# Kernel optimization log

Measured on AMD Instinct MI355X. Metric: run time of the kernel, lower is better.

Reference implementation:

```python
import jax, jax.numpy as jnp
import numpy as np
from jax import lax


def _log_g(z):
    # log of g(x) = x + 0.5 if x >= 0 else sigmoid(x)
    return jnp.where(z >= 0, jnp.log(jax.nn.relu(z) + 0.5), -jax.nn.softplus(-z))


def setup_inputs() -> dict:
    key = jax.random.key(0)
    k1, k2, k3 = jax.random.split(key, 3)
    B, S, D, H = 8, 8192, 512, 256
    x = jax.random.normal(k1, (B, S, D), dtype=jnp.float32)
    h_prev = jax.random.normal(k2, (B, H), dtype=jnp.float32)
    # nn.Linear(D, 3H, bias=False) weight: [3H, D], scaled like torch default init
    W = jax.random.normal(k3, (3 * H, D), dtype=jnp.float32) * (1.0 / np.sqrt(D))
    return {"x": x, "h_prev": h_prev, "W": W}


def reference(x, h_prev, W):
    # x: [B,S,D], h_prev: [B,H], W: [3H,D]
    seq_len = x.shape[1]
    y = jnp.einsum("bsd,hd->bsh", x, W)              # [B,S,3H]
    f, i, h = jnp.split(y, 3, axis=-1)                # each [B,S,H]
    diff = jax.nn.softplus(-f) - jax.nn.softplus(-i)
    log_f = -jax.nn.softplus(diff)                    # log(sigmoid-normalized forget gate)
    log_i = -jax.nn.softplus(-diff)                   # log(input gate)
    log_h0 = _log_g(h_prev)                           # [B,H]
    log_tilde_h = _log_g(h)                           # [B,S,H]
    # parallel scan in log space: h_t = f_t * h_{t-1} + i_t * g(h_t~)
    a_star = jnp.concatenate(
        [jnp.zeros_like(log_h0)[:, None], jnp.cumsum(log_f, axis=1)], axis=1
    )                                                  # [B,S+1,H]
    log_vals = jnp.concatenate([log_h0[:, None], log_i + log_tilde_h], axis=1)  # [B,S+1,H]
    log_h = a_star + lax.cumlogsumexp(log_vals - a_star, axis=1)
    h_t = jnp.exp(log_h)                               # [B,S+1,H]
    return h_t[:, -seq_len:]                           # [B,S,H]
```

## Files before the change

kernel.cpp:

```cpp
#include <hip/hip_runtime.h>
#include <hip/hip_fp16.h>
#include <math.h>

#define BB 8
#define SS 8192
#define DD 512
#define HH 256
#define MM (BB * SS)
#define NN 768
#define CC 256
#define LL 32

typedef unsigned short u16;
typedef __attribute__((ext_vector_type(8))) short short8;
typedef __attribute__((ext_vector_type(4))) float f32x4;

#define AS1(p) ((const __attribute__((address_space(1))) void*)(p))
#define AS3(p) ((__attribute__((address_space(3))) void*)(p))

__device__ __forceinline__ u16 f2bf_rtne(float f) {
    union { float f; unsigned u; } v; v.f = f;
    unsigned r = v.u + 0x7fffu + ((v.u >> 16) & 1u);
    return (u16)(r >> 16);
}
__device__ __forceinline__ unsigned pack2_rtn(float a, float b) {
    union { float f; unsigned u; } x, y; x.f = a; y.f = b;
    return ((x.u + 0x8000u) >> 16) | ((y.u + 0x8000u) & 0xffff0000u);
}

__device__ __forceinline__ float sp_fast(float z) {
    return (z > 15.0f) ? z : __logf(1.0f + __expf(z));
}

__device__ __forceinline__ unsigned packFu(float F, float u) {
    __half2 h = __floats2half2_rn(F, u);
    return *reinterpret_cast<unsigned*>(&h);
}
__device__ __forceinline__ float2 unpackFu(unsigned v) {
    __half2 h = *reinterpret_cast<__half2*>(&v);
    return __half22float2(h);
}

__global__ __launch_bounds__(256) void convert_W(const float* __restrict__ W,
                                                 u16* __restrict__ Wr) {
    const int chunk = blockIdx.x * 256 + threadIdx.x;
    const int kcb = chunk / 768;
    const int u = chunk % 768;
    const int kc = kcb >> 2, cb = kcb & 3;
    const int v = u & 31;
    const int s = ((v >> 2) & 7) ^ ((v >> 4) & 1);
    const int q = (v & 3) ^ (s & 3);
    const int r = ((u >> 5) << 3) | s;
    const int w = r / 48;
    const int rr = r % 48;
    const int jn = rr >> 4, hl = rr & 15;
    const int wrow = jn * HH + cb * 64 + w * 16 + hl;
    const int k0 = kc * 32 + q * 8;
    const float4 v0 = *(const float4*)&W[(size_t)wrow * DD + k0];
    const float4 v1 = *(const float4*)&W[(size_t)wrow * DD + k0 + 4];
    u16 o[8];
    o[0]=f2bf_rtne(v0.x); o[1]=f2bf_rtne(v0.y); o[2]=f2bf_rtne(v0.z); o[3]=f2bf_rtne(v0.w);
    o[4]=f2bf_rtne(v1.x); o[5]=f2bf_rtne(v1.y); o[6]=f2bf_rtne(v1.z); o[7]=f2bf_rtne(v1.w);
    *(uint4*)&Wr[(size_t)chunk * 8] = *(const uint4*)o;
}

__global__ __launch_bounds__(256, 4) void gemm_gate_mfma(
    const float* __restrict__ x,
    const u16* __restrict__ Wr,
    unsigned* __restrict__ Fu)
{
    __shared__ __align__(16) u16 Bs[2][6144];
    __shared__ __align__(16) u16 As[2][64 * 40];

    const int tid = threadIdx.x;
    const int L = (blockIdx.x & 7) * 512 + (blockIdx.x >> 3);
    const int mblk = L >> 2, cb = L & 3;
    const int m0 = mblk * 64;

    const int w = tid >> 6;
    const int lane = tid & 63;
    const int l16 = lane & 15;
    const int quad = lane >> 4;

    const int arow = tid >> 2;
    const int aqi = tid & 3;

    f32x4 acc[4][3];
    #pragma unroll
    for (int a = 0; a < 4; ++a)
        #pragma unroll
        for (int b = 0; b < 3; ++b)
            #pragma unroll
            for (int e = 0; e < 4; ++e) acc[a][b][e] = 0.0f;

    int boff[3];
    #pragma unroll
    for (int jn = 0; jn < 3; ++jn) {
        const int r = w * 48 + jn * 16 + l16;
        boff[jn] = (((r * 4 + quad) ^ (r & 7))) * 8;
    }

    const float* xrow = &x[(size_t)(m0 + arow) * DD];

    {
        const size_t ub = (size_t)(0 * 4 + cb) * 768;
        #pragma unroll
        for (int i = 0; i < 3; ++i) {
            const int idx = i * 256 + tid;
            __builtin_amdgcn_global_load_lds(AS1(Wr + (ub + idx) * 8),
                                             AS3(&Bs[0][idx * 8]), 16, 0, 0);
        }
    }
    float4 va0 = *(const float4*)&xrow[aqi * 8];
    float4 va1 = *(const float4*)&xrow[aqi * 8 + 4];
    float4 ar0 = *(const float4*)&xrow[32 + aqi * 8];
    float4 ar1 = *(const float4*)&xrow[32 + aqi * 8 + 4];
    {
        uint4 p;
        p.x = pack2_rtn(va0.x, va0.y); p.y = pack2_rtn(va0.z, va0.w);
        p.z = pack2_rtn(va1.x, va1.y); p.w = pack2_rtn(va1.z, va1.w);
        *(uint4*)&As[0][arow * 40 + aqi * 8] = p;
    }
    __syncthreads();

    for (int kc = 0; kc < 16; ++kc) {
        const int buf = kc & 1;
        if (kc < 15) {
            const size_t ub = (size_t)((kc + 1) * 4 + cb) * 768;
            #pragma unroll
            for (int i = 0; i < 3; ++i) {
                const int idx = i * 256 + tid;
                __builtin_amdgcn_global_load_lds(AS1(Wr + (ub + idx) * 8),
                                                 AS3(&Bs[buf ^ 1][idx * 8]), 16, 0, 0);
            }
            uint4 p;
            p.x = pack2_rtn(ar0.x, ar0.y); p.y = pack2_rtn(ar0.z, ar0.w);
            p.z = pack2_rtn(ar1.x, ar1.y); p.w = pack2_rtn(ar1.z, ar1.w);
            *(uint4*)&As[buf ^ 1][arow * 40 + aqi * 8] = p;
            if (kc < 14) {
                ar0 = *(const float4*)&xrow[(kc + 2) * 32 + aqi * 8];
                ar1 = *(const float4*)&xrow[(kc + 2) * 32 + aqi * 8 + 4];
            }
        }
        short8 afr[4];
        #pragma unroll
        for (int mf = 0; mf < 4; ++mf)
            afr[mf] = *(const short8*)&As[buf][(mf * 16 + l16) * 40 + quad * 8];
        short8 bfr[3];
        #pragma unroll
        for (int jn = 0; jn < 3; ++jn)
            bfr[jn] = *(const short8*)&Bs[buf][boff[jn]];

        __builtin_amdgcn_s_setprio(1);
        #pragma unroll
        for (int mf = 0; mf < 4; ++mf)
            #pragma unroll
            for (int jn = 0; jn < 3; ++jn)
                acc[mf][jn] = __builtin_amdgcn_mfma_f32_16x16x32_bf16(
                    afr[mf], bfr[jn], acc[mf][jn], 0, 0, 0);
        __builtin_amdgcn_s_setprio(0);
        __syncthreads();
    }

    const int head = cb * 64 + w * 16 + l16;
    #pragma unroll
    for (int mf = 0; mf < 4; ++mf) {
        #pragma unroll
        for (int r = 0; r < 4; ++r) {
            const int m = m0 + mf * 16 + quad * 4 + r;
            const float fr = acc[mf][0][r];
            const float ir = acc[mf][1][r];
            const float hr = acc[mf][2][r];
            const float diff = sp_fast(-fr) - sp_fast(-ir);
            const float F = __builtin_amdgcn_rcpf(1.0f + __expf(diff));
            const float I = 1.0f - F;
            const float G = (hr >= 0.0f) ? (hr + 0.5f)
                                         : __builtin_amdgcn_rcpf(1.0f + __expf(-hr));
            Fu[(size_t)m * HH + head] = packFu(F, I * G);
        }
    }
}

__global__ __launch_bounds__(256) void scan_pass1(
    const unsigned* __restrict__ Fu,
    float* __restrict__ P_arr, float* __restrict__ U_arr) {
    const int pair = blockIdx.x * 2 + (threadIdx.x >> 7);
    const int b = pair / CC;
    const int c = pair % CC;
    const int h0 = (threadIdx.x & 127) * 2;
    size_t base = ((size_t)(b * SS + c * LL)) * HH + h0;
    float P0 = 1.0f, P1 = 1.0f, U0 = 0.0f, U1 = 0.0f;
    #pragma unroll 8
    for (int t = 0; t < LL; ++t) {
        const uint2 fu = *(const uint2*)&Fu[base];
        const float2 a = unpackFu(fu.x);
        const float2 d = unpackFu(fu.y);
        U0 = a.x * U0 + a.y;  P0 *= a.x;
        U1 = d.x * U1 + d.y;  P1 *= d.x;
        base += HH;
    }
    const size_t o = ((size_t)c * BB + b) * HH + h0;
    *(float2*)&P_arr[o] = make_float2(P0, P1);
    *(float2*)&U_arr[o] = make_float2(U0, U1);
}

__global__ __launch_bounds__(256) void scan_pass2(
    const float* __restrict__ h_prev, const float* __restrict__ P_arr,
    const float* __restrict__ U_arr, float* __restrict__ Hin) {
    const int b = blockIdx.x;
    const int h = threadIdx.x;
    const float z = h_prev[b * HH + h];
    float carry = (z >= 0.0f) ? (z + 0.5f) : __builtin_amdgcn_rcpf(1.0f + __expf(-z));
    #pragma unroll 8
    for (int c = 0; c < CC; ++c) {
        const size_t o = ((size_t)c * BB + b) * HH + h;
        Hin[o] = carry;
        carry = P_arr[o] * carry + U_arr[o];
    }
}

__global__ __launch_bounds__(256) void scan_pass3(
    const float* __restrict__ Hin, unsigned* buf) {
    const int pair = blockIdx.x * 2 + (threadIdx.x >> 7);
    const int b = pair / CC;
    const int c = pair % CC;
    const int h0 = (threadIdx.x & 127) * 2;
    float2 hv = *(const float2*)&Hin[((size_t)c * BB + b) * HH + h0];
    size_t base = ((size_t)(b * SS + c * LL)) * HH + h0;
    #pragma unroll 8
    for (int t = 0; t < LL; ++t) {
        const uint2 fu = *(const uint2*)&buf[base];
        const float2 a = unpackFu(fu.x);
        const float2 d = unpackFu(fu.y);
        hv.x = a.x * hv.x + a.y;
        hv.y = d.x * hv.y + d.y;
        *(float2*)&buf[base] = hv;
        base += HH;
    }
}

extern "C" void kernel_launch(void* const* d_in, const int* in_sizes, int n_in,
                              void* d_out, int out_size, void* d_ws, size_t ws_size,
                              hipStream_t stream) {
    const float* x      = (const float*)d_in[0];
    const float* h_prev = (const float*)d_in[1];
    const float* W      = (const float*)d_in[2];

    float* P_arr = (float*)d_ws;
    float* U_arr = P_arr + (size_t)CC * BB * HH;
    float* Hin   = U_arr + (size_t)CC * BB * HH;
    u16*   Wr    = (u16*)(Hin + (size_t)CC * BB * HH);

    convert_W<<<192, 256, 0, stream>>>(W, Wr);
    gemm_gate_mfma<<<4096, 256, 0, stream>>>(x, Wr, (unsigned*)d_out);
    scan_pass1<<<BB * CC / 2, 256, 0, stream>>>((const unsigned*)d_out, P_arr, U_arr);
    scan_pass2<<<BB, 256, 0, stream>>>(h_prev, P_arr, U_arr, Hin);
    scan_pass3<<<BB * CC / 2, 256, 0, stream>>>(Hin, (unsigned*)d_out);
}
```

Baseline: 333.0 us.

## Fuse chunk scan reduction into GEMM epilogue with register-resident A fragments

The GEMM is restructured so each block keeps a full 16-head slice of W in LDS for all of K, and each wave loads its own 64 rows of x straight into registers as bf16 fragments, dropping the A shared-memory staging and per-iteration barriers. The epilogue computes each chunk's (P,U) scan summary with wave shuffles, so the separate scan_pass1 kernel and its re-read of Fu go away. Chunk length becomes 64 to match a wave's row tile. The trade-off is more LDS per block (lower occupancy bound), uncoalesced direct x loads, and no reuse of x rows across waves.

```diff
diff --git a/kernel.cpp b/kernel.cpp
--- a/kernel.cpp
+++ b/kernel.cpp
@@ -7,9 +7,8 @@
 #define DD 512
 #define HH 256
 #define MM (BB * SS)
-#define NN 768
-#define CC 256
-#define LL 32
+#define CC 128
+#define LL 64
 
 typedef unsigned short u16;
 typedef __attribute__((ext_vector_type(8))) short short8;
@@ -41,49 +40,64 @@
     return __half22float2(h);
 }
 
+__device__ __forceinline__ short8 packfrag(const float4& a, const float4& b) {
+    uint4 t;
+    t.x = pack2_rtn(a.x, a.y); t.y = pack2_rtn(a.z, a.w);
+    t.z = pack2_rtn(b.x, b.y); t.w = pack2_rtn(b.z, b.w);
+    return *reinterpret_cast<short8*>(&t);
+}
+
 __global__ __launch_bounds__(256) void convert_W(const float* __restrict__ W,
                                                  u16* __restrict__ Wr) {
-    const int chunk = blockIdx.x * 256 + threadIdx.x;
-    const int kcb = chunk / 768;
-    const int u = chunk % 768;
-    const int kc = kcb >> 2, cb = kcb & 3;
-    const int v = u & 31;
-    const int s = ((v >> 2) & 7) ^ ((v >> 4) & 1);
-    const int q = (v & 3) ^ (s & 3);
-    const int r = ((u >> 5) << 3) | s;
-    const int w = r / 48;
-    const int rr = r % 48;
-    const int jn = rr >> 4, hl = rr & 15;
-    const int wrow = jn * HH + cb * 64 + w * 16 + hl;
-    const int k0 = kc * 32 + q * 8;
+    const int idx = blockIdx.x * 256 + threadIdx.x;
+    const int nb  = idx / 3072;
+    const int rem = idx % 3072;
+    const int kc  = rem / 192;
+    const int v   = rem % 192;
+    const int r   = v >> 2, quad = v & 3;
+    const int jn = r >> 4, hl = r & 15;
+    const int wrow = jn * HH + nb * 16 + hl;
+    const int k0 = kc * 32 + quad * 8;
     const float4 v0 = *(const float4*)&W[(size_t)wrow * DD + k0];
     const float4 v1 = *(const float4*)&W[(size_t)wrow * DD + k0 + 4];
     u16 o[8];
     o[0]=f2bf_rtne(v0.x); o[1]=f2bf_rtne(v0.y); o[2]=f2bf_rtne(v0.z); o[3]=f2bf_rtne(v0.w);
     o[4]=f2bf_rtne(v1.x); o[5]=f2bf_rtne(v1.y); o[6]=f2bf_rtne(v1.z); o[7]=f2bf_rtne(v1.w);
-    *(uint4*)&Wr[(size_t)chunk * 8] = *(const uint4*)o;
-}
-
-__global__ __launch_bounds__(256, 4) void gemm_gate_mfma(
+    const int dst = nb * 3072 + kc * 192 + (v ^ (r & 7));
+    *(uint4*)&Wr[(size_t)dst * 8] = *(const uint4*)o;
+}
+
+__global__ __launch_bounds__(256, 3) void gemm_gate_mfma(
     const float* __restrict__ x,
     const u16* __restrict__ Wr,
+    float* __restrict__ P_arr,
+    float* __restrict__ U_arr,
     unsigned* __restrict__ Fu)
 {
-    __shared__ __align__(16) u16 Bs[2][6144];
-    __shared__ __align__(16) u16 As[2][64 * 40];
+    __shared__ __align__(16) u16 Bs[24576];
 
     const int tid = threadIdx.x;
-    const int L = (blockIdx.x & 7) * 512 + (blockIdx.x >> 3);
-    const int mblk = L >> 2, cb = L & 3;
-    const int m0 = mblk * 64;
-
+    const int nb   = blockIdx.x & 15;
+    const int mblk = blockIdx.x >> 4;
     const int w = tid >> 6;
     const int lane = tid & 63;
     const int l16 = lane & 15;
     const int quad = lane >> 4;
-
-    const int arow = tid >> 2;
-    const int aqi = tid & 3;
+    const int m0w = mblk * 256 + w * 64;
+
+    #pragma unroll
+    for (int i = 0; i < 12; ++i) {
+        const int u = i * 256 + tid;
+        __builtin_amdgcn_global_load_lds(AS1(Wr + ((size_t)nb * 3072 + u) * 8),
+                                         AS3(&Bs[u * 8]), 16, 0, 0);
+    }
+
+    int boff[3];
+    #pragma unroll
+    for (int jn = 0; jn < 3; ++jn) {
+        const int r = jn * 16 + l16;
+        boff[jn] = ((4 * r + quad) ^ (r & 7)) * 8;
+    }
 
     f32x4 acc[4][3];
     #pragma unroll
@@ -93,115 +107,110 @@
             #pragma unroll
             for (int e = 0; e < 4; ++e) acc[a][b][e] = 0.0f;
 
-    int boff[3];
-    #pragma unroll
-    for (int jn = 0; jn < 3; ++jn) {
-        const int r = w * 48 + jn * 16 + l16;
-        boff[jn] = (((r * 4 + quad) ^ (r & 7))) * 8;
-    }
-
-    const float* xrow = &x[(size_t)(m0 + arow) * DD];
-
-    {
-        const size_t ub = (size_t)(0 * 4 + cb) * 768;
-        #pragma unroll
-        for (int i = 0; i < 3; ++i) {
-            const int idx = i * 256 + tid;
-            __builtin_amdgcn_global_load_lds(AS1(Wr + (ub + idx) * 8),
-                                             AS3(&Bs[0][idx * 8]), 16, 0, 0);
-        }
-    }
-    float4 va0 = *(const float4*)&xrow[aqi * 8];
-    float4 va1 = *(const float4*)&xrow[aqi * 8 + 4];
-    float4 ar0 = *(const float4*)&xrow[32 + aqi * 8];
-    float4 ar1 = *(const float4*)&xrow[32 + aqi * 8 + 4];
-    {
-        uint4 p;
-        p.x = pack2_rtn(va0.x, va0.y); p.y = pack2_rtn(va0.z, va0.w);
-        p.z = pack2_rtn(va1.x, va1.y); p.w = pack2_rtn(va1.z, va1.w);
-        *(uint4*)&As[0][arow * 40 + aqi * 8] = p;
+    const float* xw = x + (size_t)m0w * DD;
+    const int aoff = l16 * DD + quad * 8;
+
+    float4 ra[4][2];
+    #pragma unroll
+    for (int mf = 0; mf < 4; ++mf) {
+        ra[mf][0] = *(const float4*)&xw[mf * 16 * DD + aoff];
+        ra[mf][1] = *(const float4*)&xw[mf * 16 * DD + aoff + 4];
     }
     __syncthreads();
 
+    short8 afrA[4], afrB[4];
+    #pragma unroll
+    for (int mf = 0; mf < 4; ++mf) afrA[mf] = packfrag(ra[mf][0], ra[mf][1]);
+
+    #pragma unroll
     for (int kc = 0; kc < 16; ++kc) {
-        const int buf = kc & 1;
         if (kc < 15) {
-            const size_t ub = (size_t)((kc + 1) * 4 + cb) * 768;
-            #pragma unroll
-            for (int i = 0; i < 3; ++i) {
-                const int idx = i * 256 + tid;
-                __builtin_amdgcn_global_load_lds(AS1(Wr + (ub + idx) * 8),
-                                                 AS3(&Bs[buf ^ 1][idx * 8]), 16, 0, 0);
+            #pragma unroll
+            for (int mf = 0; mf < 4; ++mf) {
+                ra[mf][0] = *(const float4*)&xw[mf * 16 * DD + aoff + (kc + 1) * 32];
+                ra[mf][1] = *(const float4*)&xw[mf * 16 * DD + aoff + (kc + 1) * 32 + 4];
             }
-            uint4 p;
-            p.x = pack2_rtn(ar0.x, ar0.y); p.y = pack2_rtn(ar0.z, ar0.w);
-            p.z = pack2_rtn(ar1.x, ar1.y); p.w = pack2_rtn(ar1.z, ar1.w);
-            *(uint4*)&As[buf ^ 1][arow * 40 + aqi * 8] = p;
-            if (kc < 14) {
-                ar0 = *(const float4*)&xrow[(kc + 2) * 32 + aqi * 8];
-                ar1 = *(const float4*)&xrow[(kc + 2) * 32 + aqi * 8 + 4];
-            }
-        }
-        short8 afr[4];
-        #pragma unroll
-        for (int mf = 0; mf < 4; ++mf)
-            afr[mf] = *(const short8*)&As[buf][(mf * 16 + l16) * 40 + quad * 8];
+        }
         short8 bfr[3];
         #pragma unroll
         for (int jn = 0; jn < 3; ++jn)
-            bfr[jn] = *(const short8*)&Bs[buf][boff[jn]];
+            bfr[jn] = *(const short8*)&Bs[kc * 1536 + boff[jn]];
 
         __builtin_amdgcn_s_setprio(1);
-        #pragma unroll
-        for (int mf = 0; mf < 4; ++mf)
-            #pragma unroll
-            for (int jn = 0; jn < 3; ++jn)
-                acc[mf][jn] = __builtin_amdgcn_mfma_f32_16x16x32_bf16(
-                    afr[mf], bfr[jn], acc[mf][jn], 0, 0, 0);
+        if ((kc & 1) == 0) {
+            #pragma unroll
+            for (int mf = 0; mf < 4; ++mf)
+                #pragma unroll
+                for (int jn = 0; jn < 3; ++jn)
+                    acc[mf][jn] = __builtin_amdgcn_mfma_f32_16x16x32_bf16(
+                        afrA[mf], bfr[jn], acc[mf][jn], 0, 0, 0);
+        } else {
+            #pragma unroll
+            for (int mf = 0; mf < 4; ++mf)
+                #pragma unroll
+                for (int jn = 0; jn < 3; ++jn)
+                    acc[mf][jn] = __builtin_amdgcn_mfma_f32_16x16x32_bf16(
+                        afrB[mf], bfr[jn], acc[mf][jn], 0, 0, 0);
+        }
         __builtin_amdgcn_s_setprio(0);
-        __syncthreads();
-    }
-
-    const int head = cb * 64 + w * 16 + l16;
+
+        if (kc < 15) {
+            if ((kc & 1) == 0) {
+                #pragma unroll
+                for (int mf = 0; mf < 4; ++mf) afrB[mf] = packfrag(ra[mf][0], ra[mf][1]);
+            } else {
+                #pragma unroll
+                for (int mf = 0; mf < 4; ++mf) afrA[mf] = packfrag(ra[mf][0], ra[mf][1]);
+            }
+        }
+    }
+
+    const int head = nb * 16 + l16;
+    const int bI = m0w >> 13;
+    const int cI = (m0w >> 6) & (CC - 1);
+    float Pt = 1.0f, Ut = 0.0f;
     #pragma unroll
     for (int mf = 0; mf < 4; ++mf) {
+        float Pseg = 1.0f, Useg = 0.0f;
         #pragma unroll
         for (int r = 0; r < 4; ++r) {
-            const int m = m0 + mf * 16 + quad * 4 + r;
             const float fr = acc[mf][0][r];
             const float ir = acc[mf][1][r];
             const float hr = acc[mf][2][r];
             const float diff = sp_fast(-fr) - sp_fast(-ir);
             const float F = __builtin_amdgcn_rcpf(1.0f + __expf(diff));
-            const float I = 1.0f - F;
             const float G = (hr >= 0.0f) ? (hr + 0.5f)
                                          : __builtin_amdgcn_rcpf(1.0f + __expf(-hr));
-            Fu[(size_t)m * HH + head] = packFu(F, I * G);
-        }
-    }
-}
-
-__global__ __launch_bounds__(256) void scan_pass1(
-    const unsigned* __restrict__ Fu,
-    float* __restrict__ P_arr, float* __restrict__ U_arr) {
-    const int pair = blockIdx.x * 2 + (threadIdx.x >> 7);
-    const int b = pair / CC;
-    const int c = pair % CC;
-    const int h0 = (threadIdx.x & 127) * 2;
-    size_t base = ((size_t)(b * SS + c * LL)) * HH + h0;
-    float P0 = 1.0f, P1 = 1.0f, U0 = 0.0f, U1 = 0.0f;
-    #pragma unroll 8
-    for (int t = 0; t < LL; ++t) {
-        const uint2 fu = *(const uint2*)&Fu[base];
-        const float2 a = unpackFu(fu.x);
-        const float2 d = unpackFu(fu.y);
-        U0 = a.x * U0 + a.y;  P0 *= a.x;
-        U1 = d.x * U1 + d.y;  P1 *= d.x;
-        base += HH;
-    }
-    const size_t o = ((size_t)c * BB + b) * HH + h0;
-    *(float2*)&P_arr[o] = make_float2(P0, P1);
-    *(float2*)&U_arr[o] = make_float2(U0, U1);
+            const unsigned pw = packFu(F, (1.0f - F) * G);
+            Fu[(size_t)(m0w + mf * 16 + quad * 4 + r) * HH + head] = pw;
+            const float2 q = unpackFu(pw);
+            Useg = q.x * Useg + q.y;
+            Pseg *= q.x;
+        }
+        {
+            const float Pp = __shfl_xor(Pseg, 16);
+            const float Up = __shfl_xor(Useg, 16);
+            const bool hi = (quad & 1);
+            const float Plo = hi ? Pp : Pseg, Ulo = hi ? Up : Useg;
+            const float Phi = hi ? Pseg : Pp, Uhi = hi ? Useg : Up;
+            Pseg = Plo * Phi;  Useg = Phi * Ulo + Uhi;
+        }
+        {
+            const float Pp = __shfl_xor(Pseg, 32);
+            const float Up = __shfl_xor(Useg, 32);
+            const bool hi = (quad & 2);
+            const float Plo = hi ? Pp : Pseg, Ulo = hi ? Up : Useg;
+            const float Phi = hi ? Pseg : Pp, Uhi = hi ? Useg : Up;
+            Pseg = Plo * Phi;  Useg = Phi * Ulo + Uhi;
+        }
+        Ut = Pseg * Ut + Useg;
+        Pt *= Pseg;
+    }
+    if (quad == 0) {
+        const size_t o = ((size_t)cI * BB + bI) * HH + head;
+        P_arr[o] = Pt;
+        U_arr[o] = Ut;
+    }
 }
 
 __global__ __launch_bounds__(256) void scan_pass2(
@@ -252,8 +261,7 @@
     u16*   Wr    = (u16*)(Hin + (size_t)CC * BB * HH);
 
     convert_W<<<192, 256, 0, stream>>>(W, Wr);
-    gemm_gate_mfma<<<4096, 256, 0, stream>>>(x, Wr, (unsigned*)d_out);
-    scan_pass1<<<BB * CC / 2, 256, 0, stream>>>((const unsigned*)d_out, P_arr, U_arr);
+    gemm_gate_mfma<<<4096, 256, 0, stream>>>(x, Wr, P_arr, U_arr, (unsigned*)d_out);
     scan_pass2<<<BB, 256, 0, stream>>>(h_prev, P_arr, U_arr, Hin);
     scan_pass3<<<BB * CC / 2, 256, 0, stream>>>(Hin, (unsigned*)d_out);
 }
```

Measured after the change: 462.1 us. +38.8%, slower.
